# Optimization experiments

Measured on AMD Instinct MI355X. Metric: run time of the kernel, lower is better.

The kernel has to match this reference:

```python
import jax, jax.numpy as jnp
import numpy as np

NEG_SLOPE = 0.2  # PyG GATConv default LeakyReLU negative slope
NUM_GRAPHS = 256


def gat_conv(x, edge_src, edge_dst, W, att_src, att_dst, bias):
    """PyG-style GATConv. x:[N,Fin], W:[H*C,Fin], att_*:[H,C], bias:[H*C]."""
    N = x.shape[0]
    H, C = att_src.shape
    h = (x @ W.T).reshape(N, H, C)                       # [N,H,C]
    a_src = jnp.sum(h * att_src, axis=-1)                # [N,H]
    a_dst = jnp.sum(h * att_dst, axis=-1)                # [N,H]
    e = jax.nn.leaky_relu(a_src[edge_src] + a_dst[edge_dst], NEG_SLOPE)  # [E,H]
    # segment softmax over edges sharing the same destination node
    m = jax.ops.segment_max(e, edge_dst, num_segments=N)
    ex = jnp.exp(e - m[edge_dst])
    den = jax.ops.segment_sum(ex, edge_dst, num_segments=N)
    alpha = ex / (den[edge_dst] + 1e-16)                 # [E,H]
    out = jax.ops.segment_sum(h[edge_src] * alpha[..., None], edge_dst,
                              num_segments=N)            # [N,H,C]
    return out.reshape(N, H * C) + bias


def setup_inputs() -> dict:
    key = jax.random.key(0)
    ks = jax.random.split(key, 16)
    N, E, Fin = 20000, 320000, 128
    H1, C1 = 8, 64          # conv1: heads=8, hidden_dim1=64 -> concat 512
    D1 = H1 * C1            # 512
    D2 = 128                # hidden_dim2, conv2 heads=1
    OUT = 2
    s = lambda k, shp, fan: jax.random.normal(k, shp, jnp.float32) * (1.0 / np.sqrt(fan))
    x = jax.random.normal(ks[0], (N, Fin), jnp.float32)
    edge_index = jax.random.randint(ks[1], (2, E), 0, N, jnp.int32)
    batch = jnp.sort(jax.random.randint(ks[2], (N,), 0, NUM_GRAPHS, jnp.int32))
    return {
        "x": x, "edge_index": edge_index, "batch": batch,
        "W1": s(ks[3], (D1, Fin), Fin), "att_src1": s(ks[4], (H1, C1), C1),
        "att_dst1": s(ks[5], (H1, C1), C1), "b1": jnp.zeros((D1,), jnp.float32),
        "W2": s(ks[6], (D2, D1), D1), "att_src2": s(ks[7], (1, D2), D2),
        "att_dst2": s(ks[8], (1, D2), D2), "b2": jnp.zeros((D2,), jnp.float32),
        "w_attn": s(ks[9], (D2, 1), D2), "b_attn": jnp.zeros((1,), jnp.float32),
        "w_mask": s(ks[10], (D2, 1), D2), "b_mask": jnp.zeros((1,), jnp.float32),
        "W_out": s(ks[11], (OUT, D2), D2), "b_out": jnp.zeros((OUT,), jnp.float32),
    }


def reference(x, edge_index, batch, W1, att_src1, att_dst1, b1,
              W2, att_src2, att_dst2, b2, w_attn, b_attn, w_mask, b_mask,
              W_out, b_out):
    N = x.shape[0]
    loops = jnp.arange(N, dtype=edge_index.dtype)
    src = jnp.concatenate([edge_index[0], loops])  # PyG add_self_loops=True
    dst = jnp.concatenate([edge_index[1], loops])

    h = gat_conv(x, src, dst, W1, att_src1, att_dst1, b1)   # [N, 512]
    h = jax.nn.relu(h)                                      # dropout = identity (eval)
    h = gat_conv(h, src, dst, W2, att_src2, att_dst2, b2)   # [N, 128]
    h = jax.nn.relu(h)

    # attention pooling over graphs in the batch
    attn_scores = h @ w_attn + b_attn                       # [N,1]
    node_mask = jax.nn.sigmoid(h @ w_mask + b_mask)         # [N,1]
    weighted = h * (attn_scores * node_mask)                # [N,128]
    pooled = jax.ops.segment_sum(weighted, batch, num_segments=NUM_GRAPHS)
    return pooled @ W_out.T + b_out                         # [256, 2]
```

## Files before the change

### kernel.cpp

```cpp
#include <hip/hip_runtime.h>
#include <math.h>


#define NEG_SLOPE 0.2f

using bf16x8 = __attribute__((ext_vector_type(8))) __bf16;
using f32x4  = __attribute__((ext_vector_type(4))) float;

__device__ __forceinline__ ushort f2bf(float f) {
    unsigned u = __float_as_uint(f);
    unsigned r = (u + 0x7FFFu + ((u >> 16) & 1u)) >> 16;
    return (ushort)r;
}
__device__ __forceinline__ unsigned pack2(float a, float b) {
    return (unsigned)f2bf(a) | ((unsigned)f2bf(b) << 16);
}
__device__ __forceinline__ float bflo(unsigned u) { return __uint_as_float(u << 16); }
__device__ __forceinline__ float bfhi(unsigned u) { return __uint_as_float(u & 0xFFFF0000u); }
__device__ __forceinline__ void unpack8(uint4 u, float* f) {
    f[0] = bflo(u.x); f[1] = bfhi(u.x);
    f[2] = bflo(u.y); f[3] = bfhi(u.y);
    f[4] = bflo(u.z); f[5] = bfhi(u.z);
    f[6] = bflo(u.w); f[7] = bfhi(u.w);
}
__device__ __forceinline__ void unpack4(uint2 u, float* f) {
    f[0] = bflo(u.x); f[1] = bfhi(u.x);
    f[2] = bflo(u.y); f[3] = bfhi(u.y);
}

__global__ __launch_bounds__(256) void cvt3(const float* __restrict__ x, ushort* __restrict__ xb, int nx4,
                                            const float* __restrict__ w1, ushort* __restrict__ w1b, int nw14,
                                            const float* __restrict__ w2, ushort* __restrict__ w2b, int nw24) {
    int i = blockIdx.x * 256 + threadIdx.x;
    const float* src; ushort* dst; int j = i;
    if (j < nx4) { src = x; dst = xb; }
    else {
        j -= nx4;
        if (j < nw14) { src = w1; dst = w1b; }
        else {
            j -= nw14;
            if (j >= nw24) return;
            src = w2; dst = w2b;
        }
    }
    float4 v = ((const float4*)src)[j];
    uint2 o;
    o.x = pack2(v.x, v.y);
    o.y = pack2(v.z, v.w);
    ((uint2*)dst)[j] = o;
}

#define LDSB 40
__global__ __launch_bounds__(256) void gemm_mfma(const ushort* __restrict__ A,
                                                 const ushort* __restrict__ B,
                                                 ushort* __restrict__ C,
                                                 int M, int N, int K,
                                                 const float* __restrict__ att_s,
                                                 const float* __restrict__ att_d,
                                                 float* __restrict__ sout,
                                                 float* __restrict__ dout,
                                                 int H) {
    __shared__ ushort As[128 * LDSB];
    __shared__ ushort Bs[128 * LDSB];
    int t = threadIdx.x;
    int wave = t >> 6, lane = t & 63;
    int quad = lane >> 4, l16 = lane & 15;
    int m0 = blockIdx.x * 128;
    int n0 = blockIdx.y * 128;
    int wm = (wave & 1) * 64;
    int wn = (wave >> 1) * 64;
    int srow = t >> 1;
    int sseg = (t & 1) * 16;
    f32x4 acc[4][4] = {};
    for (int k0 = 0; k0 < K; k0 += 32) {
        uint4 av0, av1, bv0, bv1;
        {
            int grow = m0 + srow;
            if (grow < M) {
                const uint4* gp = (const uint4*)(A + (size_t)grow * K + k0 + sseg);
                av0 = gp[0]; av1 = gp[1];
            } else {
                av0 = make_uint4(0, 0, 0, 0); av1 = av0;
            }
            const uint4* gq = (const uint4*)(B + (size_t)(n0 + srow) * K + k0 + sseg);
            bv0 = gq[0]; bv1 = gq[1];
        }
        __syncthreads();
        *(uint4*)&As[srow * LDSB + sseg]     = av0;
        *(uint4*)&As[srow * LDSB + sseg + 8] = av1;
        *(uint4*)&Bs[srow * LDSB + sseg]     = bv0;
        *(uint4*)&Bs[srow * LDSB + sseg + 8] = bv1;
        __syncthreads();
        bf16x8 af[4], bf[4];
#pragma unroll
        for (int i = 0; i < 4; ++i)
            af[i] = *(const bf16x8*)&As[(wm + i * 16 + l16) * LDSB + quad * 8];
#pragma unroll
        for (int j = 0; j < 4; ++j)
            bf[j] = *(const bf16x8*)&Bs[(wn + j * 16 + l16) * LDSB + quad * 8];
#pragma unroll
        for (int i = 0; i < 4; ++i)
#pragma unroll
            for (int j = 0; j < 4; ++j)
                acc[i][j] = __builtin_amdgcn_mfma_f32_16x16x32_bf16(
                    af[i], bf[j], acc[i][j], 0, 0, 0);
    }
#pragma unroll
    for (int i = 0; i < 4; ++i) {
#pragma unroll
        for (int r = 0; r < 4; ++r) {
            int grow = m0 + wm + i * 16 + quad * 4 + r;
            if (grow < M) {
#pragma unroll
                for (int j = 0; j < 4; ++j) {
                    int gcol = n0 + wn + j * 16 + l16;
                    C[(size_t)grow * N + gcol] = f2bf(acc[i][j][r]);
                }
            }
        }
    }
    float as[4], adw[4];
#pragma unroll
    for (int j = 0; j < 4; ++j) {
        int col = n0 + wn + j * 16 + l16;
        as[j]  = att_s[col];
        adw[j] = att_d[col];
    }
    int head = (H == 8) ? ((n0 + wn) >> 6) : 0;
#pragma unroll
    for (int i = 0; i < 4; ++i) {
#pragma unroll
        for (int r = 0; r < 4; ++r) {
            float ps = acc[i][0][r] * as[0] + acc[i][1][r] * as[1] +
                       acc[i][2][r] * as[2] + acc[i][3][r] * as[3];
            float pd = acc[i][0][r] * adw[0] + acc[i][1][r] * adw[1] +
                       acc[i][2][r] * adw[2] + acc[i][3][r] * adw[3];
#pragma unroll
            for (int off = 1; off < 16; off <<= 1) {
                ps += __shfl_xor(ps, off);
                pd += __shfl_xor(pd, off);
            }
            int grow = m0 + wm + i * 16 + quad * 4 + r;
            if (l16 == 0 && grow < M) {
                if (H == 1) {
                    atomicAdd(&sout[grow], ps);
                    atomicAdd(&dout[grow], pd);
                } else {
                    sout[grow * 8 + head] = ps;
                    dout[grow * 8 + head] = pd;
                }
            }
        }
    }
}

__global__ void count_edges(const int* __restrict__ dst, int* cnt, int E) {
    int e = blockIdx.x * 256 + threadIdx.x;
    if (e < E) atomicAdd(&cnt[dst[e]], 1);
}

__global__ __launch_bounds__(1024) void scan_offsets(const int* cnt, int* row_start,
                                                     int* cursor, int N) {
    __shared__ int sm[1024];
    int t = threadIdx.x;
    int per = (N + 1023) / 1024;
    int beg = t * per;
    int end = beg + per; if (end > N) end = N;
    int sum = 0;
    for (int i = beg; i < end; ++i) sum += cnt[i];
    sm[t] = sum;
    __syncthreads();
    for (int off = 1; off < 1024; off <<= 1) {
        int add = (t >= off) ? sm[t - off] : 0;
        __syncthreads();
        sm[t] += add;
        __syncthreads();
    }
    int run = sm[t] - sum;
    for (int i = beg; i < end; ++i) {
        int c = cnt[i];
        row_start[i] = run;
        cursor[i] = run;
        run += c;
    }
    if (t == 1023) row_start[N] = run;
}

__global__ void fill_edges(const int* __restrict__ src, const int* __restrict__ dst,
                           int* cursor, int* __restrict__ srcs, int E) {
    int e = blockIdx.x * 256 + threadIdx.x;
    if (e < E) {
        int pos = atomicAdd(&cursor[dst[e]], 1);
        srcs[pos] = src[e];
    }
}

__global__ __launch_bounds__(256) void agg1(const ushort* __restrict__ h1,
                                            const float* __restrict__ a1s,
                                            const float* __restrict__ a1d,
                                            const int* __restrict__ row_start,
                                            const int* __restrict__ srcs,
                                            const float* __restrict__ b1,
                                            ushort* __restrict__ r1, int N) {
    int node = blockIdx.x * 4 + (threadIdx.x >> 6);
    if (node >= N) return;
    int lane = threadIdx.x & 63;
    int head = lane >> 3;
    int f0 = lane * 8;
    int pbeg = row_start[node], pend = row_start[node + 1];
    float ad = a1d[node * 8 + head];
    float es = a1s[node * 8 + head] + ad;
    es = es > 0.f ? es : NEG_SLOPE * es;
    float ex_self = __expf(es);
    float den = ex_self;
    float q[8];
    unpack8(*(const uint4*)(h1 + (size_t)node * 512 + f0), q);
    float acc[8];
#pragma unroll
    for (int j = 0; j < 8; ++j) acc[j] = ex_self * q[j];
    for (int p = pbeg; p < pend; p += 8) {
        int sidx[8]; bool okb[8];
#pragma unroll
        for (int k = 0; k < 8; ++k) {
            int pk = p + k;
            okb[k] = pk < pend;
            sidx[k] = srcs[okb[k] ? pk : pbeg];
        }
        uint4 u[8];
#pragma unroll
        for (int k = 0; k < 8; ++k)
            u[k] = *(const uint4*)(h1 + (size_t)sidx[k] * 512 + f0);
        float sc[8];
#pragma unroll
        for (int k = 0; k < 8; ++k) sc[k] = a1s[sidx[k] * 8 + head];
#pragma unroll
        for (int k = 0; k < 8; ++k) {
            float e = sc[k] + ad;
            e = e > 0.f ? e : NEG_SLOPE * e;
            float xk = okb[k] ? __expf(e) : 0.f;
            den += xk;
            float v[8];
            unpack8(u[k], v);
#pragma unroll
            for (int j = 0; j < 8; ++j) acc[j] += xk * v[j];
        }
    }
    float rden = 1.0f / (den + 1e-16f);
    const float4* bp = (const float4*)(b1 + f0);
    float4 b0 = bp[0], b1v = bp[1];
    float o[8];
    o[0] = fmaxf(acc[0] * rden + b0.x, 0.f);
    o[1] = fmaxf(acc[1] * rden + b0.y, 0.f);
    o[2] = fmaxf(acc[2] * rden + b0.z, 0.f);
    o[3] = fmaxf(acc[3] * rden + b0.w, 0.f);
    o[4] = fmaxf(acc[4] * rden + b1v.x, 0.f);
    o[5] = fmaxf(acc[5] * rden + b1v.y, 0.f);
    o[6] = fmaxf(acc[6] * rden + b1v.z, 0.f);
    o[7] = fmaxf(acc[7] * rden + b1v.w, 0.f);
    uint4 ov;
    ov.x = pack2(o[0], o[1]); ov.y = pack2(o[2], o[3]);
    ov.z = pack2(o[4], o[5]); ov.w = pack2(o[6], o[7]);
    *(uint4*)(r1 + (size_t)node * 512 + f0) = ov;
}

__global__ __launch_bounds__(256) void agg2(const ushort* __restrict__ h2,
                                            const float* __restrict__ a2s,
                                            const float* __restrict__ a2d,
                                            const int* __restrict__ row_start,
                                            const int* __restrict__ srcs,
                                            const float* __restrict__ b2,
                                            float* __restrict__ r2, int N) {
    int node = blockIdx.x * 8 + (threadIdx.x >> 5);
    if (node >= N) return;
    int sub = threadIdx.x & 31;
    int f0 = sub * 4;
    int pbeg = row_start[node], pend = row_start[node + 1];
    float ad = a2d[node];
    float es = a2s[node] + ad;
    es = es > 0.f ? es : NEG_SLOPE * es;
    float ex_self = __expf(es);
    float den = ex_self;
    float q[4];
    unpack4(*(const uint2*)(h2 + (size_t)node * 128 + f0), q);
    float acc[4];
#pragma unroll
    for (int j = 0; j < 4; ++j) acc[j] = ex_self * q[j];
    int p = pbeg;
    for (; p + 4 <= pend; p += 4) {
        int s0 = srcs[p + 0];
        int s1 = srcs[p + 1];
        int s2 = srcs[p + 2];
        int s3 = srcs[p + 3];
        uint2 u0 = *(const uint2*)(h2 + (size_t)s0 * 128 + f0);
        uint2 u1 = *(const uint2*)(h2 + (size_t)s1 * 128 + f0);
        uint2 u2 = *(const uint2*)(h2 + (size_t)s2 * 128 + f0);
        uint2 u3 = *(const uint2*)(h2 + (size_t)s3 * 128 + f0);
        float as0 = a2s[s0];
        float as1 = a2s[s1];
        float as2 = a2s[s2];
        float as3 = a2s[s3];
        float e0 = as0 + ad; e0 = e0 > 0.f ? e0 : NEG_SLOPE * e0;
        float e1 = as1 + ad; e1 = e1 > 0.f ? e1 : NEG_SLOPE * e1;
        float e2 = as2 + ad; e2 = e2 > 0.f ? e2 : NEG_SLOPE * e2;
        float e3 = as3 + ad; e3 = e3 > 0.f ? e3 : NEG_SLOPE * e3;
        float x0 = __expf(e0), x1 = __expf(e1), x2 = __expf(e2), x3 = __expf(e3);
        den += (x0 + x1) + (x2 + x3);
        float v[4];
        unpack4(u0, v);
#pragma unroll
        for (int j = 0; j < 4; ++j) acc[j] += x0 * v[j];
        unpack4(u1, v);
#pragma unroll
        for (int j = 0; j < 4; ++j) acc[j] += x1 * v[j];
        unpack4(u2, v);
#pragma unroll
        for (int j = 0; j < 4; ++j) acc[j] += x2 * v[j];
        unpack4(u3, v);
#pragma unroll
        for (int j = 0; j < 4; ++j) acc[j] += x3 * v[j];
    }
    for (; p < pend; ++p) {
        int s = srcs[p];
        float e = a2s[s] + ad;
        e = e > 0.f ? e : NEG_SLOPE * e;
        float ex = __expf(e);
        den += ex;
        float v[4];
        unpack4(*(const uint2*)(h2 + (size_t)s * 128 + f0), v);
#pragma unroll
        for (int j = 0; j < 4; ++j) acc[j] += ex * v[j];
    }
    float rden = 1.0f / (den + 1e-16f);
    float4 bv = *(const float4*)(b2 + f0);
    float4 o;
    o.x = fmaxf(acc[0] * rden + bv.x, 0.f);
    o.y = fmaxf(acc[1] * rden + bv.y, 0.f);
    o.z = fmaxf(acc[2] * rden + bv.z, 0.f);
    o.w = fmaxf(acc[3] * rden + bv.w, 0.f);
    *(float4*)(r2 + (size_t)node * 128 + f0) = o;
}

__global__ __launch_bounds__(256) void pool_kernel(const float* __restrict__ r2,
                                                   const int* __restrict__ batch,
                                                   const float* __restrict__ w_attn,
                                                   const float* __restrict__ b_attn,
                                                   const float* __restrict__ w_mask,
                                                   const float* __restrict__ b_mask,
                                                   float* pooled, int N) {
    int node = blockIdx.x * 4 + (threadIdx.x >> 6);
    if (node >= N) return;
    int lane = threadIdx.x & 63;
    float2 h = *(const float2*)(r2 + (size_t)node * 128 + lane * 2);
    float2 wa = *(const float2*)(w_attn + lane * 2);
    float2 wm = *(const float2*)(w_mask + lane * 2);
    float pa = h.x * wa.x + h.y * wa.y;
    float pm = h.x * wm.x + h.y * wm.y;
#pragma unroll
    for (int off = 1; off < 64; off <<= 1) {
        pa += __shfl_xor(pa, off);
        pm += __shfl_xor(pm, off);
    }
    float attn = pa + b_attn[0];
    float mask = 1.0f / (1.0f + __expf(-(pm + b_mask[0])));
    float w = attn * mask;
    int g = batch[node];
    atomicAdd(&pooled[g * 128 + lane * 2], h.x * w);
    atomicAdd(&pooled[g * 128 + lane * 2 + 1], h.y * w);
}

__global__ void final_kernel(const float* __restrict__ pooled,
                             const float* __restrict__ W_out,
                             const float* __restrict__ b_out,
                             float* __restrict__ out) {
    int tid = blockIdx.x * 256 + threadIdx.x;
    if (tid >= 512) return;
    int g = tid >> 1, o = tid & 1;
    const float* p = pooled + g * 128;
    const float* w = W_out + o * 128;
    float s = 0.f;
#pragma unroll 4
    for (int f = 0; f < 128; ++f) s += p[f] * w[f];
    out[tid] = s + b_out[o];
}

extern "C" void kernel_launch(void* const* d_in, const int* in_sizes, int n_in,
                              void* d_out, int out_size, void* d_ws, size_t ws_size,
                              hipStream_t stream) {
    const float* x        = (const float*)d_in[0];
    const int* edge_index = (const int*)d_in[1];
    const int* batch      = (const int*)d_in[2];
    const float* W1       = (const float*)d_in[3];
    const float* att_src1 = (const float*)d_in[4];
    const float* att_dst1 = (const float*)d_in[5];
    const float* b1       = (const float*)d_in[6];
    const float* W2       = (const float*)d_in[7];
    const float* att_src2 = (const float*)d_in[8];
    const float* att_dst2 = (const float*)d_in[9];
    const float* b2       = (const float*)d_in[10];
    const float* w_attn   = (const float*)d_in[11];
    const float* b_attn   = (const float*)d_in[12];
    const float* w_mask   = (const float*)d_in[13];
    const float* b_mask   = (const float*)d_in[14];
    const float* W_out    = (const float*)d_in[15];
    const float* b_out    = (const float*)d_in[16];
    float* out = (float*)d_out;

    int N = in_sizes[0] / 128;
    int E = in_sizes[1] / 2;
    const int* esrc = edge_index;
    const int* edst = edge_index + E;

    char* ws = (char*)d_ws;
    size_t off = 0;
    auto alloc = [&](size_t bytes) {
        void* p = ws + off;
        off = (off + bytes + 255) & ~(size_t)255;
        return p;
    };
    ushort* h1       = (ushort*)alloc((size_t)N * 512 * 2);
    ushort* r1       = (ushort*)alloc((size_t)N * 512 * 2);
    ushort* h2       = (ushort*)alloc((size_t)N * 128 * 2);
    float*  r2       = (float*)alloc((size_t)N * 128 * 4);
    ushort* xb       = (ushort*)alloc((size_t)N * 128 * 2);
    ushort* w1b      = (ushort*)alloc((size_t)512 * 128 * 2);
    ushort* w2b      = (ushort*)alloc((size_t)128 * 512 * 2);
    float*  a1s      = (float*)alloc((size_t)N * 8 * 4);
    float*  a1d      = (float*)alloc((size_t)N * 8 * 4);
    int*    row_start= (int*)alloc((size_t)(N + 1) * 4);
    int*    srcs     = (int*)alloc((size_t)E * 4);
    int*    cursor   = (int*)alloc((size_t)N * 4);
    float*  a2s      = (float*)alloc((size_t)N * 4);
    float*  a2d      = (float*)alloc((size_t)N * 4);
    float*  pooled   = (float*)alloc((size_t)256 * 128 * 4);
    size_t zspan = (size_t)((char*)(pooled + 256 * 128) - (char*)cursor);
    hipMemsetAsync(cursor, 0, zspan, stream);

    dim3 b256(256);
    int nx4 = N * 128 / 4;
    int nw4 = 512 * 128 / 4;
    cvt3<<<(nx4 + 2 * nw4 + 255) / 256, b256, 0, stream>>>(x, xb, nx4, W1, w1b, nw4,
                                                           W2, w2b, nw4);
    count_edges<<<(E + 255) / 256, b256, 0, stream>>>(edst, cursor, E);
    scan_offsets<<<1, 1024, 0, stream>>>(cursor, row_start, cursor, N);
    fill_edges<<<(E + 255) / 256, b256, 0, stream>>>(esrc, edst, cursor, srcs, E);
    gemm_mfma<<<dim3((N + 127) / 128, 512 / 128), b256, 0, stream>>>(
        xb, w1b, h1, N, 512, 128, att_src1, att_dst1, a1s, a1d, 8);
    agg1<<<(N + 3) / 4, b256, 0, stream>>>(h1, a1s, a1d, row_start, srcs, b1, r1, N);
    gemm_mfma<<<dim3((N + 127) / 128, 128 / 128), b256, 0, stream>>>(
        r1, w2b, h2, N, 128, 512, att_src2, att_dst2, a2s, a2d, 1);
    agg2<<<(N + 7) / 8, b256, 0, stream>>>(h2, a2s, a2d, row_start, srcs, b2, r2, N);
    pool_kernel<<<(N + 3) / 4, b256, 0, stream>>>(r2, batch, w_attn, b_attn, w_mask,
                                                  b_mask, pooled, N);
    final_kernel<<<2, b256, 0, stream>>>(pooled, W_out, b_out, out);
}
```

Before: 294.1 us.

## Fuse launches, prefetch GEMM tiles, fuse pooling into layer-2 aggregation

```diff
diff --git a/kernel.cpp b/kernel.cpp
--- a/kernel.cpp
+++ b/kernel.cpp
@@ -3,6 +3,7 @@
 
 
 #define NEG_SLOPE 0.2f
+#define LDSB 40
 
 using bf16x8 = __attribute__((ext_vector_type(8))) __bf16;
 using f32x4  = __attribute__((ext_vector_type(4))) float;
@@ -28,69 +29,81 @@
     f[2] = bflo(u.y); f[3] = bfhi(u.y);
 }
 
-__global__ __launch_bounds__(256) void cvt3(const float* __restrict__ x, ushort* __restrict__ xb, int nx4,
+__global__ __launch_bounds__(256) void prep(const float* __restrict__ x, ushort* __restrict__ xb, int nx4,
                                             const float* __restrict__ w1, ushort* __restrict__ w1b, int nw14,
-                                            const float* __restrict__ w2, ushort* __restrict__ w2b, int nw24) {
-    int i = blockIdx.x * 256 + threadIdx.x;
-    const float* src; ushort* dst; int j = i;
-    if (j < nx4) { src = x; dst = xb; }
-    else {
-        j -= nx4;
-        if (j < nw14) { src = w1; dst = w1b; }
+                                            const float* __restrict__ w2, ushort* __restrict__ w2b, int nw24,
+                                            int cvtBlocks,
+                                            const int* __restrict__ edst, int* __restrict__ cnt, int E) {
+    int blk = blockIdx.x;
+    if (blk < cvtBlocks) {
+        int j = blk * 256 + threadIdx.x;
+        const float* src; ushort* dst;
+        if (j < nx4) { src = x; dst = xb; }
         else {
-            j -= nw14;
-            if (j >= nw24) return;
-            src = w2; dst = w2b;
+            j -= nx4;
+            if (j < nw14) { src = w1; dst = w1b; }
+            else {
+                j -= nw14;
+                if (j >= nw24) return;
+                src = w2; dst = w2b;
+            }
         }
-    }
-    float4 v = ((const float4*)src)[j];
-    uint2 o;
-    o.x = pack2(v.x, v.y);
-    o.y = pack2(v.z, v.w);
-    ((uint2*)dst)[j] = o;
-}
-
-#define LDSB 40
-__global__ __launch_bounds__(256) void gemm_mfma(const ushort* __restrict__ A,
-                                                 const ushort* __restrict__ B,
-                                                 ushort* __restrict__ C,
-                                                 int M, int N, int K,
-                                                 const float* __restrict__ att_s,
-                                                 const float* __restrict__ att_d,
-                                                 float* __restrict__ sout,
-                                                 float* __restrict__ dout,
-                                                 int H) {
-    __shared__ ushort As[128 * LDSB];
-    __shared__ ushort Bs[128 * LDSB];
+        float4 v = ((const float4*)src)[j];
+        uint2 o;
+        o.x = pack2(v.x, v.y);
+        o.y = pack2(v.z, v.w);
+        ((uint2*)dst)[j] = o;
+    } else {
+        int e = (blk - cvtBlocks) * 256 + threadIdx.x;
+        if (e < E) atomicAdd(&cnt[edst[e]], 1);
+    }
+}
+
+__device__ __forceinline__ void gemm_body(ushort* As, ushort* Bs,
+                                          const ushort* __restrict__ A,
+                                          const ushort* __restrict__ B,
+                                          ushort* __restrict__ C,
+                                          int M, int N, int K, int bx, int by,
+                                          const float* __restrict__ att_s,
+                                          const float* __restrict__ att_d,
+                                          float* __restrict__ sout,
+                                          float* __restrict__ dout, int H) {
     int t = threadIdx.x;
     int wave = t >> 6, lane = t & 63;
     int quad = lane >> 4, l16 = lane & 15;
-    int m0 = blockIdx.x * 128;
-    int n0 = blockIdx.y * 128;
+    int m0 = bx * 128, n0 = by * 128;
     int wm = (wave & 1) * 64;
     int wn = (wave >> 1) * 64;
     int srow = t >> 1;
     int sseg = (t & 1) * 16;
+    int growA = m0 + srow;
+    bool okA = growA < M;
     f32x4 acc[4][4] = {};
+    uint4 av0, av1, bv0, bv1;
+    {
+        if (okA) {
+            const uint4* gp = (const uint4*)(A + (size_t)growA * K + sseg);
+            av0 = gp[0]; av1 = gp[1];
+        } else { av0 = make_uint4(0, 0, 0, 0); av1 = av0; }
+        const uint4* gq = (const uint4*)(B + (size_t)(n0 + srow) * K + sseg);
+        bv0 = gq[0]; bv1 = gq[1];
+    }
     for (int k0 = 0; k0 < K; k0 += 32) {
-        uint4 av0, av1, bv0, bv1;
-        {
-            int grow = m0 + srow;
-            if (grow < M) {
-                const uint4* gp = (const uint4*)(A + (size_t)grow * K + k0 + sseg);
-                av0 = gp[0]; av1 = gp[1];
-            } else {
-                av0 = make_uint4(0, 0, 0, 0); av1 = av0;
-            }
-            const uint4* gq = (const uint4*)(B + (size_t)(n0 + srow) * K + k0 + sseg);
-            bv0 = gq[0]; bv1 = gq[1];
-        }
         __syncthreads();
         *(uint4*)&As[srow * LDSB + sseg]     = av0;
         *(uint4*)&As[srow * LDSB + sseg + 8] = av1;
         *(uint4*)&Bs[srow * LDSB + sseg]     = bv0;
         *(uint4*)&Bs[srow * LDSB + sseg + 8] = bv1;
         __syncthreads();
+        int k1 = k0 + 32;
+        if (k1 < K) {
+            if (okA) {
+                const uint4* gp = (const uint4*)(A + (size_t)growA * K + k1 + sseg);
+                av0 = gp[0]; av1 = gp[1];
+            } else { av0 = make_uint4(0, 0, 0, 0); av1 = av0; }
+            const uint4* gq = (const uint4*)(B + (size_t)(n0 + srow) * K + k1 + sseg);
+            bv0 = gq[0]; bv1 = gq[1];
+        }
         bf16x8 af[4], bf[4];
 #pragma unroll
         for (int i = 0; i < 4; ++i)
@@ -154,9 +167,47 @@
     }
 }
 
-__global__ void count_edges(const int* __restrict__ dst, int* cnt, int E) {
-    int e = blockIdx.x * 256 + threadIdx.x;
-    if (e < E) atomicAdd(&cnt[dst[e]], 1);
+__global__ __launch_bounds__(256) void g1f(const ushort* __restrict__ A,
+                                           const ushort* __restrict__ B,
+                                           ushort* __restrict__ C,
+                                           int M, int N, int K,
+                                           const float* __restrict__ att_s,
+                                           const float* __restrict__ att_d,
+                                           float* __restrict__ sout,
+                                           float* __restrict__ dout, int H,
+                                           int gemmBlocks, int nby,
+                                           const int* __restrict__ esrc,
+                                           const int* __restrict__ edst,
+                                           int* __restrict__ cursor,
+                                           int* __restrict__ srcs, int E) {
+    __shared__ ushort As[128 * LDSB];
+    __shared__ ushort Bs[128 * LDSB];
+    int blk = blockIdx.x;
+    if (blk < gemmBlocks) {
+        gemm_body(As, Bs, A, B, C, M, N, K, blk / nby, blk % nby,
+                  att_s, att_d, sout, dout, H);
+    } else {
+        int e = (blk - gemmBlocks) * 256 + threadIdx.x;
+        if (e < E) {
+            int pos = atomicAdd(&cursor[edst[e]], 1);
+            srcs[pos] = esrc[e];
+        }
+    }
+}
+
+__global__ __launch_bounds__(256) void gemm_k(const ushort* __restrict__ A,
+                                              const ushort* __restrict__ B,
+                                              ushort* __restrict__ C,
+                                              int M, int N, int K,
+                                              const float* __restrict__ att_s,
+                                              const float* __restrict__ att_d,
+                                              float* __restrict__ sout,
+                                              float* __restrict__ dout, int H,
+                                              int nby) {
+    __shared__ ushort As[128 * LDSB];
+    __shared__ ushort Bs[128 * LDSB];
+    gemm_body(As, Bs, A, B, C, M, N, K, blockIdx.x / nby, blockIdx.x % nby,
+              att_s, att_d, sout, dout, H);
 }
 
 __global__ __launch_bounds__(1024) void scan_offsets(const int* cnt, int* row_start,
@@ -184,15 +235,6 @@
         run += c;
     }
     if (t == 1023) row_start[N] = run;
-}
-
-__global__ void fill_edges(const int* __restrict__ src, const int* __restrict__ dst,
-                           int* cursor, int* __restrict__ srcs, int E) {
-    int e = blockIdx.x * 256 + threadIdx.x;
-    if (e < E) {
-        int pos = atomicAdd(&cursor[dst[e]], 1);
-        srcs[pos] = src[e];
-    }
 }
 
 __global__ __launch_bounds__(256) void agg1(const ushort* __restrict__ h1,
@@ -218,32 +260,50 @@
     float acc[8];
 #pragma unroll
     for (int j = 0; j < 8; ++j) acc[j] = ex_self * q[j];
-    for (int p = pbeg; p < pend; p += 8) {
-        int sidx[8]; bool okb[8];
-#pragma unroll
-        for (int k = 0; k < 8; ++k) {
-            int pk = p + k;
-            okb[k] = pk < pend;
-            sidx[k] = srcs[okb[k] ? pk : pbeg];
-        }
-        uint4 u[8];
-#pragma unroll
-        for (int k = 0; k < 8; ++k)
-            u[k] = *(const uint4*)(h1 + (size_t)sidx[k] * 512 + f0);
-        float sc[8];
-#pragma unroll
-        for (int k = 0; k < 8; ++k) sc[k] = a1s[sidx[k] * 8 + head];
-#pragma unroll
-        for (int k = 0; k < 8; ++k) {
-            float e = sc[k] + ad;
-            e = e > 0.f ? e : NEG_SLOPE * e;
-            float xk = okb[k] ? __expf(e) : 0.f;
-            den += xk;
-            float v[8];
-            unpack8(u[k], v);
-#pragma unroll
-            for (int j = 0; j < 8; ++j) acc[j] += xk * v[j];
-        }
+    int p = pbeg;
+    for (; p + 4 <= pend; p += 4) {
+        int s0 = srcs[p + 0];
+        int s1 = srcs[p + 1];
+        int s2 = srcs[p + 2];
+        int s3 = srcs[p + 3];
+        uint4 u0 = *(const uint4*)(h1 + (size_t)s0 * 512 + f0);
+        uint4 u1 = *(const uint4*)(h1 + (size_t)s1 * 512 + f0);
+        uint4 u2 = *(const uint4*)(h1 + (size_t)s2 * 512 + f0);
+        uint4 u3 = *(const uint4*)(h1 + (size_t)s3 * 512 + f0);
+        float as0 = a1s[s0 * 8 + head];
+        float as1 = a1s[s1 * 8 + head];
+        float as2 = a1s[s2 * 8 + head];
+        float as3 = a1s[s3 * 8 + head];
+        float e0 = as0 + ad; e0 = e0 > 0.f ? e0 : NEG_SLOPE * e0;
+        float e1 = as1 + ad; e1 = e1 > 0.f ? e1 : NEG_SLOPE * e1;
+        float e2 = as2 + ad; e2 = e2 > 0.f ? e2 : NEG_SLOPE * e2;
+        float e3 = as3 + ad; e3 = e3 > 0.f ? e3 : NEG_SLOPE * e3;
+        float x0 = __expf(e0), x1 = __expf(e1), x2 = __expf(e2), x3 = __expf(e3);
+        den += (x0 + x1) + (x2 + x3);
+        float v[8];
+        unpack8(u0, v);
+#pragma unroll
+        for (int j = 0; j < 8; ++j) acc[j] += x0 * v[j];
+        unpack8(u1, v);
+#pragma unroll
+        for (int j = 0; j < 8; ++j) acc[j] += x1 * v[j];
+        unpack8(u2, v);
+#pragma unroll
+        for (int j = 0; j < 8; ++j) acc[j] += x2 * v[j];
+        unpack8(u3, v);
+#pragma unroll
+        for (int j = 0; j < 8; ++j) acc[j] += x3 * v[j];
+    }
+    for (; p < pend; ++p) {
+        int s = srcs[p];
+        float e = a1s[s * 8 + head] + ad;
+        e = e > 0.f ? e : NEG_SLOPE * e;
+        float ex = __expf(e);
+        den += ex;
+        float v[8];
+        unpack8(*(const uint4*)(h1 + (size_t)s * 512 + f0), v);
+#pragma unroll
+        for (int j = 0; j < 8; ++j) acc[j] += ex * v[j];
     }
     float rden = 1.0f / (den + 1e-16f);
     const float4* bp = (const float4*)(b1 + f0);
@@ -263,13 +323,18 @@
     *(uint4*)(r1 + (size_t)node * 512 + f0) = ov;
 }
 
-__global__ __launch_bounds__(256) void agg2(const ushort* __restrict__ h2,
-                                            const float* __restrict__ a2s,
-                                            const float* __restrict__ a2d,
-                                            const int* __restrict__ row_start,
-                                            const int* __restrict__ srcs,
-                                            const float* __restrict__ b2,
-                                            float* __restrict__ r2, int N) {
+__global__ __launch_bounds__(256) void agg2pool(const ushort* __restrict__ h2,
+                                                const float* __restrict__ a2s,
+                                                const float* __restrict__ a2d,
+                                                const int* __restrict__ row_start,
+                                                const int* __restrict__ srcs,
+                                                const float* __restrict__ b2,
+                                                const int* __restrict__ batch,
+                                                const float* __restrict__ w_attn,
+                                                const float* __restrict__ b_attn,
+                                                const float* __restrict__ w_mask,
+                                                const float* __restrict__ b_mask,
+                                                float* __restrict__ pooled, int N) {
     int node = blockIdx.x * 8 + (threadIdx.x >> 5);
     if (node >= N) return;
     int sub = threadIdx.x & 31;
@@ -337,26 +402,12 @@
     o.y = fmaxf(acc[1] * rden + bv.y, 0.f);
     o.z = fmaxf(acc[2] * rden + bv.z, 0.f);
     o.w = fmaxf(acc[3] * rden + bv.w, 0.f);
-    *(float4*)(r2 + (size_t)node * 128 + f0) = o;
-}
-
-__global__ __launch_bounds__(256) void pool_kernel(const float* __restrict__ r2,
-                                                   const int* __restrict__ batch,
-                                                   const float* __restrict__ w_attn,
-                                                   const float* __restrict__ b_attn,
-                                                   const float* __restrict__ w_mask,
-                                                   const float* __restrict__ b_mask,
-                                                   float* pooled, int N) {
-    int node = blockIdx.x * 4 + (threadIdx.x >> 6);
-    if (node >= N) return;
-    int lane = threadIdx.x & 63;
-    float2 h = *(const float2*)(r2 + (size_t)node * 128 + lane * 2);
-    float2 wa = *(const float2*)(w_attn + lane * 2);
-    float2 wm = *(const float2*)(w_mask + lane * 2);
-    float pa = h.x * wa.x + h.y * wa.y;
-    float pm = h.x * wm.x + h.y * wm.y;
-#pragma unroll
-    for (int off = 1; off < 64; off <<= 1) {
+    float4 wa = *(const float4*)(w_attn + f0);
+    float4 wm = *(const float4*)(w_mask + f0);
+    float pa = o.x * wa.x + o.y * wa.y + o.z * wa.z + o.w * wa.w;
+    float pm = o.x * wm.x + o.y * wm.y + o.z * wm.z + o.w * wm.w;
+#pragma unroll
+    for (int off = 1; off < 32; off <<= 1) {
         pa += __shfl_xor(pa, off);
         pm += __shfl_xor(pm, off);
     }
@@ -364,8 +415,11 @@
     float mask = 1.0f / (1.0f + __expf(-(pm + b_mask[0])));
     float w = attn * mask;
     int g = batch[node];
-    atomicAdd(&pooled[g * 128 + lane * 2], h.x * w);
-    atomicAdd(&pooled[g * 128 + lane * 2 + 1], h.y * w);
+    float* pg = pooled + (size_t)g * 128 + f0;
+    atomicAdd(pg + 0, o.x * w);
+    atomicAdd(pg + 1, o.y * w);
+    atomicAdd(pg + 2, o.z * w);
+    atomicAdd(pg + 3, o.w * w);
 }
 
 __global__ void final_kernel(const float* __restrict__ pooled,
@@ -420,7 +474,6 @@
     ushort* h1       = (ushort*)alloc((size_t)N * 512 * 2);
     ushort* r1       = (ushort*)alloc((size_t)N * 512 * 2);
     ushort* h2       = (ushort*)alloc((size_t)N * 128 * 2);
-    float*  r2       = (float*)alloc((size_t)N * 128 * 4);
     ushort* xb       = (ushort*)alloc((size_t)N * 128 * 2);
     ushort* w1b      = (ushort*)alloc((size_t)512 * 128 * 2);
     ushort* w2b      = (ushort*)alloc((size_t)128 * 512 * 2);
@@ -438,18 +491,22 @@
     dim3 b256(256);
     int nx4 = N * 128 / 4;
     int nw4 = 512 * 128 / 4;
-    cvt3<<<(nx4 + 2 * nw4 + 255) / 256, b256, 0, stream>>>(x, xb, nx4, W1, w1b, nw4,
-                                                           W2, w2b, nw4);
-    count_edges<<<(E + 255) / 256, b256, 0, stream>>>(edst, cursor, E);
+    int cvtBlocks = (nx4 + 2 * nw4 + 255) / 256;
+    int cntBlocks = (E + 255) / 256;
+    prep<<<cvtBlocks + cntBlocks, b256, 0, stream>>>(x, xb, nx4, W1, w1b, nw4,
+                                                     W2, w2b, nw4, cvtBlocks,
+                                                     edst, cursor, E);
     scan_offsets<<<1, 1024, 0, stream>>>(cursor, row_start, cursor, N);
-    fill_edges<<<(E + 255) / 256, b256, 0, stream>>>(esrc, edst, cursor, srcs, E);
-    gemm_mfma<<<dim3((N + 127) / 128, 512 / 128), b256, 0, stream>>>(
-        xb, w1b, h1, N, 512, 128, att_src1, att_dst1, a1s, a1d, 8);
+    int g1Blocks = ((N + 127) / 128) * 4;
+    g1f<<<g1Blocks + cntBlocks, b256, 0, stream>>>(xb, w1b, h1, N, 512, 128,
+                                                   att_src1, att_dst1, a1s, a1d, 8,
+                                                   g1Blocks, 4,
+                                                   esrc, edst, cursor, srcs, E);
     agg1<<<(N + 3) / 4, b256, 0, stream>>>(h1, a1s, a1d, row_start, srcs, b1, r1, N);
-    gemm_mfma<<<dim3((N + 127) / 128, 128 / 128), b256, 0, stream>>>(
-        r1, w2b, h2, N, 128, 512, att_src2, att_dst2, a2s, a2d, 1);
-    agg2<<<(N + 7) / 8, b256, 0, stream>>>(h2, a2s, a2d, row_start, srcs, b2, r2, N);
-    pool_kernel<<<(N + 3) / 4, b256, 0, stream>>>(r2, batch, w_attn, b_attn, w_mask,
-                                                  b_mask, pooled, N);
+    gemm_k<<<(N + 127) / 128, b256, 0, stream>>>(r1, w2b, h2, N, 128, 512,
+                                                 att_src2, att_dst2, a2s, a2d, 1, 1);
+    agg2pool<<<(N + 7) / 8, b256, 0, stream>>>(h2, a2s, a2d, row_start, srcs, b2,
+                                               batch, w_attn, b_attn, w_mask, b_mask,
+                                               pooled, N);
     final_kernel<<<2, b256, 0, stream>>>(pooled, W_out, b_out, out);
 }
```

Result: no change. 291.1 us (-1.0%).
